# Kernel tuning notes

Hardware: AMD Instinct MI355X
Metric: run time of the kernel (lower is better)

## Reference

```python
import jax, jax.numpy as jnp
import numpy as np
from jax import lax

GRID_SIZE = 3


def setup_inputs() -> dict:
    key = jax.random.key(0)
    k1, k2, k3 = jax.random.split(key, 3)
    B, Cin, Cout, H, W, KH, KW, G = 32, 64, 64, 64, 64, 3, 3, GRID_SIZE
    x = jax.random.normal(k1, (B, Cin, H, W), dtype=jnp.float32)
    scale_base = jax.random.normal(k2, (Cout, Cin, KH, KW), dtype=jnp.float32) * 0.1
    scale_spline = jnp.ones((Cout, Cin, KH, KW), dtype=jnp.float32)
    coeff = jax.random.normal(k3, (2, Cout, Cin, KH, KW, G), dtype=jnp.float32) * 0.02
    bias = jnp.zeros((Cout,), dtype=jnp.float32)
    return {"x": x, "scale_base": scale_base, "scale_spline": scale_spline, "coeff": coeff, "bias": bias}


def _conv(x, w, padding=1):
    return lax.conv_general_dilated(
        x, w, window_strides=(1, 1), padding=((padding, padding), (padding, padding)),
        dimension_numbers=("NCHW", "OIHW", "NCHW"))


def reference(x, scale_base, scale_spline, coeff, bias):
    B, Cin, H, W = x.shape
    Cout, _, KH, KW = scale_base.shape
    G = coeff.shape[-1]
    # Fourier feature expansion: cos(k*x), sin(k*x) for k = 1..G
    ks = jnp.arange(1, G + 1, dtype=x.dtype)
    xk = x[:, :, None] * ks[None, None, :, None, None]          # (B, Cin, G, H, W)
    feats = jnp.concatenate([jnp.cos(xk), jnp.sin(xk)], axis=2)  # (B, Cin, 2G, H, W)
    feats = feats.reshape(B, Cin * 2 * G, H, W)
    # Spline weights: coeff (2, Cout, Cin, KH, KW, G) scaled per-tap -> (Cout, Cin*2G, KH, KW)
    w = coeff * scale_spline[None, :, :, :, :, None]
    w = jnp.transpose(w, (1, 2, 0, 5, 3, 4)).reshape(Cout, Cin * 2 * G, KH, KW)
    # Base branch: SiLU(x) convolved with scale_base
    base = jax.nn.silu(x)
    out = _conv(base, scale_base) + _conv(feats, w)
    out = out + bias[None, :, None, None]
    return out
```

## Files before the change

kernel.cpp:

```cpp
#include <hip/hip_runtime.h>

typedef __attribute__((ext_vector_type(8))) short bf16x8;
typedef __attribute__((ext_vector_type(4))) float f32x4;

#define FROW   4224
#define FBUF   42240
#define BB0    (2 * FBUF)
#define BB1    (2 * FBUF + 4096)
#define LDS_TOT (2 * FBUF + 2 * 4096)

static __device__ __forceinline__ unsigned short f2bf(float f) {
  union { float f; unsigned u; } v; v.f = f;
  unsigned r = v.u + 0x7fffu + ((v.u >> 16) & 1u);
  return (unsigned short)(r >> 16);
}

static __device__ __forceinline__ void gload16(const void* g, void* l) {
  __builtin_amdgcn_global_load_lds(
      (const __attribute__((address_space(1))) void*)g,
      (__attribute__((address_space(3))) void*)l, 16, 0, 0);
}

__global__ void pack_w_k(const float* __restrict__ sb, const float* __restrict__ ss,
                         const float* __restrict__ cf, unsigned short* __restrict__ wpk) {
  int idx = blockIdx.x * 256 + threadIdx.x;
  if (idx >= 126 * 64 * 32) return;
  int e = idx & 7;
  int q = (idx >> 3) & 3;
  int co = (idx >> 5) & 63;
  int rest = idx >> 11;
  int tap = rest % 9;
  int c2 = rest / 9;
  int c = c2 >> 1, half = c2 & 1;
  int ci = half * 32 + q * 8 + e;
  int kh = tap / 3, kw = tap % 3;
  int wi = ((co * 64 + ci) * 3 + kh) * 3 + kw;
  float v;
  if (c == 0) {
    v = sb[wi];
  } else {
    int s = (c - 1) / 3, g = (c - 1) % 3;
    v = cf[(s * 36864 + wi) * 3 + g] * ss[wi];
  }
  wpk[((c2 * 9 + tap) * 64 + co) * 32 + ((q ^ ((co >> 1) & 3)) << 3) + e] = f2bf(v);
}

__global__ void feats_k(const float* __restrict__ x, unsigned short* __restrict__ fg) {
  __shared__ __align__(16) unsigned short lds[64 * 456];
  const int b = blockIdx.x, h = blockIdx.y;
  const int tid = threadIdx.x;
  const int w = tid & 63, cig = tid >> 6;
  const int key = ((w + 1) >> 1) & 3;
  const int base = w * 456;
#pragma unroll
  for (int i = 0; i < 16; ++i) {
    int ci = cig * 16 + i;
    float v = x[(((size_t)b * 64 + ci) * 64 + h) * 64 + w];
    float sg = 1.0f / (1.0f + __expf(-v));
    float f0 = v * sg;
    float s1, c1;
    __sincosf(v, &s1, &c1);
    float c2v = c1 * c1 - s1 * s1, s2v = 2.0f * s1 * c1;
    float c3v = c1 * c2v - s1 * s2v, s3v = s1 * c2v + c1 * s2v;
    int q = ci >> 3;
    int half = q >> 2, qq = q & 3;
    int sl = (half * 4 + (qq ^ key)) * 8 + (ci & 7);
    lds[base + 0 * 64 + sl] = f2bf(f0);
    lds[base + 1 * 64 + sl] = f2bf(c1);
    lds[base + 2 * 64 + sl] = f2bf(c2v);
    lds[base + 3 * 64 + sl] = f2bf(c3v);
    lds[base + 4 * 64 + sl] = f2bf(s1);
    lds[base + 5 * 64 + sl] = f2bf(s2v);
    lds[base + 6 * 64 + sl] = f2bf(s3v);
  }
  __syncthreads();
#pragma unroll
  for (int k = 0; k < 14; ++k) {
    int u = tid + k * 256;
    int qs = u & 3;
    int ww = (u >> 2) & 63;
    int c2i = u >> 8;
    int cc = c2i >> 1, half = c2i & 1;
    uint4 v = *(const uint4*)&lds[ww * 456 + cc * 64 + (half * 4 + qs) * 8];
    unsigned short* dst = fg + ((size_t)(c2i * 32 + b) * 64 + h) * 2048 + (ww * 4 + qs) * 8;
    *(uint4*)dst = v;
  }
}

__global__ __launch_bounds__(512, 2) void gemm_k(
    const unsigned short* __restrict__ fg, const unsigned short* __restrict__ wpk,
    const float* __restrict__ bias, float* __restrict__ out) {
  extern __shared__ __align__(16) char smem[];
  const int b = blockIdx.x;
  const int h0 = blockIdx.y * 8;
  const int tid = threadIdx.x;
  const int lane = tid & 63;
  const int wid = tid >> 6;
  const int l15 = lane & 15;
  const int lg = lane >> 4;
  const char* fgB = (const char*)fg;
  const char* wpkB = (const char*)wpk;

  for (int i = tid; i < 2 * FBUF / 4; i += 512) {
    int off = i * 4;
    int off2 = (off >= FBUF) ? off - FBUF : off;
    int row = off2 / FROW;
    int cb = off2 - row * FROW;
    int hh = h0 - 1 + row;
    bool staged = ((unsigned)hh < 64u) && (cb >= 64) && (cb < 4160);
    if (!staged) ((int*)smem)[i] = 0;
  }

  for (int k = wid; k < 40; k += 8) {
    int row = k >> 2, j = k & 3;
    int hh = h0 - 1 + row;
    if ((unsigned)hh < 64u)
      gload16(fgB + ((size_t)(b * 64 + hh)) * 4096 + j * 1024 + lane * 16,
              smem + row * FROW + 64 + j * 1024);
  }
  if (wid < 4)
    gload16(wpkB + wid * 1024 + lane * 16, smem + BB0 + wid * 1024);
  __syncthreads();

  f32x4 acc[4][4];
#pragma unroll
  for (int mf = 0; mf < 4; ++mf)
#pragma unroll
    for (int nf = 0; nf < 4; ++nf)
#pragma unroll
      for (int qq = 0; qq < 4; ++qq) acc[mf][nf][qq] = 0.0f;

  for (int c2 = 0; c2 < 14; ++c2) {
    const char* f = smem + ((c2 & 1) ? FBUF : 0);
    char* fnext = smem + (((c2 + 1) & 1) ? FBUF : 0);
#pragma unroll
    for (int tap = 0; tap < 9; ++tap) {
      const int it = c2 * 9 + tap;
      if (tap < 8 && c2 < 13) {
#pragma unroll
        for (int i = 0; i < 5; ++i) {
          int k = tap * 5 + i;
          if ((k & 7) == wid) {
            int row = k >> 2, j = k & 3;
            int hh = h0 - 1 + row;
            if ((unsigned)hh < 64u)
              gload16(fgB + ((size_t)((c2 + 1) * 2048 + b * 64 + hh)) * 4096 +
                          j * 1024 + lane * 16,
                      fnext + row * FROW + 64 + j * 1024);
          }
        }
      }
      if (it < 125 && wid < 4)
        gload16(wpkB + (size_t)(it + 1) * 4096 + wid * 1024 + lane * 16,
                smem + (((it + 1) & 1) ? BB1 : BB0) + wid * 1024);

      const char* bb = smem + ((it & 1) ? BB1 : BB0);
      const int kh = tap / 3, kw = tap - kh * 3;
      const int lrow = wid + kh;

      bf16x8 A[4], Bv[4];
#pragma unroll
      for (int mf = 0; mf < 4; ++mf) {
        int col = mf * 16 + l15 + kw;
        A[mf] = *(const bf16x8*)(f + (lrow * 66 + col) * 64 + ((lg ^ ((col >> 1) & 3)) << 4));
      }
#pragma unroll
      for (int nf = 0; nf < 4; ++nf) {
        int co = nf * 16 + l15;
        Bv[nf] = *(const bf16x8*)(bb + co * 64 + ((lg ^ ((co >> 1) & 3)) << 4));
      }
#pragma unroll
      for (int mf = 0; mf < 4; ++mf)
#pragma unroll
        for (int nf = 0; nf < 4; ++nf)
          acc[mf][nf] = __builtin_amdgcn_mfma_f32_16x16x32_bf16(
              A[mf], Bv[nf], acc[mf][nf], 0, 0, 0);
      __syncthreads();
    }
  }

  const int h = h0 + wid;
#pragma unroll
  for (int mf = 0; mf < 4; ++mf) {
    int w4 = mf * 16 + (lg << 2);
#pragma unroll
    for (int nf = 0; nf < 4; ++nf) {
      int co = nf * 16 + l15;
      float bv = bias[co];
      f32x4 v = acc[mf][nf];
      f32x4 res;
      res[0] = v[0] + bv; res[1] = v[1] + bv; res[2] = v[2] + bv; res[3] = v[3] + bv;
      *(f32x4*)(out + ((size_t)(b * 64 + co) * 64 + h) * 64 + w4) = res;
    }
  }
}

__global__ void naive_k(const float* __restrict__ x, const float* __restrict__ sb,
                        const float* __restrict__ ss, const float* __restrict__ cf,
                        const float* __restrict__ bias, float* __restrict__ out) {
  int idx = blockIdx.x * 256 + threadIdx.x;
  if (idx >= 32 * 64 * 64 * 64) return;
  int w = idx & 63, h = (idx >> 6) & 63, co = (idx >> 12) & 63, b = idx >> 18;
  float acc = bias[co];
  for (int ci = 0; ci < 64; ++ci) {
    for (int kh = 0; kh < 3; ++kh) {
      int hh = h + kh - 1;
      if ((unsigned)hh >= 64u) continue;
      for (int kw = 0; kw < 3; ++kw) {
        int ww = w + kw - 1;
        if ((unsigned)ww >= 64u) continue;
        float v = x[((b * 64 + ci) * 64 + hh) * 64 + ww];
        int wi = ((co * 64 + ci) * 3 + kh) * 3 + kw;
        float s1, c1; __sincosf(v, &s1, &c1);
        float c2 = c1 * c1 - s1 * s1, s2 = 2.f * s1 * c1;
        float c3 = c1 * c2 - s1 * s2, s3 = s1 * c2 + c1 * s2;
        float t = sb[wi] * (v / (1.f + __expf(-v)));
        t += ss[wi] * (cf[wi * 3] * c1 + cf[wi * 3 + 1] * c2 + cf[wi * 3 + 2] * c3 +
                       cf[(36864 + wi) * 3] * s1 + cf[(36864 + wi) * 3 + 1] * s2 +
                       cf[(36864 + wi) * 3 + 2] * s3);
        acc += t;
      }
    }
  }
  out[idx] = acc;
}

extern "C" void kernel_launch(void* const* d_in, const int* in_sizes, int n_in,
                              void* d_out, int out_size, void* d_ws, size_t ws_size,
                              hipStream_t stream) {
  const float* x = (const float*)d_in[0];
  const float* sb = (const float*)d_in[1];
  const float* ss = (const float*)d_in[2];
  const float* cf = (const float*)d_in[3];
  const float* bias = (const float*)d_in[4];
  float* out = (float*)d_out;

  const size_t FEATS_OFF = 1u << 20;
  const size_t NEED = FEATS_OFF + (size_t)14 * 32 * 64 * 4096;
  if (ws_size >= NEED) {
    unsigned short* wpk = (unsigned short*)d_ws;
    unsigned short* fg = (unsigned short*)((char*)d_ws + FEATS_OFF);
    pack_w_k<<<1008, 256, 0, stream>>>(sb, ss, cf, wpk);
    feats_k<<<dim3(32, 64), 256, 0, stream>>>(x, fg);
    hipFuncSetAttribute((const void*)gemm_k,
                        hipFuncAttributeMaxDynamicSharedMemorySize, LDS_TOT);
    gemm_k<<<dim3(32, 8), 512, LDS_TOT, stream>>>(fg, wpk, bias, out);
  } else {
    naive_k<<<32768, 256, 0, stream>>>(x, sb, ss, cf, bias, out);
  }
}
```

Before: 107.4 us.

## Stage all nine weight taps per channel group and sync once per group

The GEMM loop now loads the features and all nine tap weight slices for the next channel group into double-buffered LDS at the start of each group. It synchronises once per channel group instead of after every tap, cutting barriers from 126 to 14. In exchange the LDS footprint rises to about 158 KB. Prefetches are also issued in one burst rather than spread across taps, which may give less even overlap of loads with compute.

```diff
diff --git a/kernel.cpp b/kernel.cpp
--- a/kernel.cpp
+++ b/kernel.cpp
@@ -5,9 +5,8 @@
 
 #define FROW   4224
 #define FBUF   42240
-#define BB0    (2 * FBUF)
-#define BB1    (2 * FBUF + 4096)
-#define LDS_TOT (2 * FBUF + 2 * 4096)
+#define BGRP   36864
+#define LDS_TOT (2 * FBUF + 2 * BGRP)
 
 static __device__ __forceinline__ unsigned short f2bf(float f) {
   union { float f; unsigned u; } v; v.f = f;
@@ -111,15 +110,24 @@
     if (!staged) ((int*)smem)[i] = 0;
   }
 
-  for (int k = wid; k < 40; k += 8) {
-    int row = k >> 2, j = k & 3;
-    int hh = h0 - 1 + row;
-    if ((unsigned)hh < 64u)
-      gload16(fgB + ((size_t)(b * 64 + hh)) * 4096 + j * 1024 + lane * 16,
-              smem + row * FROW + 64 + j * 1024);
-  }
-  if (wid < 4)
-    gload16(wpkB + wid * 1024 + lane * 16, smem + BB0 + wid * 1024);
+#define STAGE_GRP(cn, fdst, bdst)                                                \
+  for (int u = wid; u < 76; u += 8) {                                            \
+    if (u < 40) {                                                                \
+      int row = u >> 2, j = u & 3;                                               \
+      int hh = h0 - 1 + row;                                                     \
+      if ((unsigned)hh < 64u)                                                    \
+        gload16(fgB + ((size_t)((cn) * 2048 + b * 64 + hh)) * 4096 +             \
+                    j * 1024 + lane * 16,                                        \
+                (fdst) + row * FROW + 64 + j * 1024);                            \
+    } else {                                                                     \
+      int t = u - 40;                                                            \
+      int tap = t >> 2, part = t & 3;                                            \
+      gload16(wpkB + (size_t)((cn) * 9 + tap) * 4096 + part * 1024 + lane * 16,  \
+              (bdst) + tap * 4096 + part * 1024);                                \
+    }                                                                            \
+  }
+
+  STAGE_GRP(0, smem, smem + 2 * FBUF);
   __syncthreads();
 
   f32x4 acc[4][4];
@@ -131,32 +139,19 @@
       for (int qq = 0; qq < 4; ++qq) acc[mf][nf][qq] = 0.0f;
 
   for (int c2 = 0; c2 < 14; ++c2) {
-    const char* f = smem + ((c2 & 1) ? FBUF : 0);
-    char* fnext = smem + (((c2 + 1) & 1) ? FBUF : 0);
+    const int cur = c2 & 1;
+    char* f = smem + (cur ? FBUF : 0);
+    char* bgc = smem + 2 * FBUF + (cur ? BGRP : 0);
+    if (c2 < 13) {
+      char* fnext = smem + (cur ? 0 : FBUF);
+      char* bnext = smem + 2 * FBUF + (cur ? 0 : BGRP);
+      STAGE_GRP(c2 + 1, fnext, bnext);
+    }
 #pragma unroll
     for (int tap = 0; tap < 9; ++tap) {
-      const int it = c2 * 9 + tap;
-      if (tap < 8 && c2 < 13) {
-#pragma unroll
-        for (int i = 0; i < 5; ++i) {
-          int k = tap * 5 + i;
-          if ((k & 7) == wid) {
-            int row = k >> 2, j = k & 3;
-            int hh = h0 - 1 + row;
-            if ((unsigned)hh < 64u)
-              gload16(fgB + ((size_t)((c2 + 1) * 2048 + b * 64 + hh)) * 4096 +
-                          j * 1024 + lane * 16,
-                      fnext + row * FROW + 64 + j * 1024);
-          }
-        }
-      }
-      if (it < 125 && wid < 4)
-        gload16(wpkB + (size_t)(it + 1) * 4096 + wid * 1024 + lane * 16,
-                smem + (((it + 1) & 1) ? BB1 : BB0) + wid * 1024);
-
-      const char* bb = smem + ((it & 1) ? BB1 : BB0);
       const int kh = tap / 3, kw = tap - kh * 3;
       const int lrow = wid + kh;
+      const char* bb = bgc + tap * 4096;
 
       bf16x8 A[4], Bv[4];
 #pragma unroll
@@ -175,9 +170,10 @@
         for (int nf = 0; nf < 4; ++nf)
           acc[mf][nf] = __builtin_amdgcn_mfma_f32_16x16x32_bf16(
               A[mf], Bv[nf], acc[mf][nf], 0, 0, 0);
-      __syncthreads();
-    }
-  }
+    }
+    __syncthreads();
+  }
+#undef STAGE_GRP
 
   const int h = h0 + wid;
 #pragma unroll
@@ -242,8 +238,8 @@
     unsigned short* fg = (unsigned short*)((char*)d_ws + FEATS_OFF);
     pack_w_k<<<1008, 256, 0, stream>>>(sb, ss, cf, wpk);
     feats_k<<<dim3(32, 64), 256, 0, stream>>>(x, fg);
-    hipFuncSetAttribute((const void*)gemm_k,
-                        hipFuncAttributeMaxDynamicSharedMemorySize, LDS_TOT);
+    (void)hipFuncSetAttribute((const void*)gemm_k,
+                              hipFuncAttributeMaxDynamicSharedMemorySize, LDS_TOT);
     gemm_k<<<dim3(32, 8), 512, LDS_TOT, stream>>>(fg, wpk, bias, out);
   } else {
     naive_k<<<32768, 256, 0, stream>>>(x, sb, ss, cf, bias, out);
```

New measurement: 98.19 us. 1.09x faster.
